# Kernel tuning notes

Measured on AMD Instinct MI355X. Metric: run time of the kernel, lower is better.

Reference implementation:

```python
import jax, jax.numpy as jnp
import numpy as np

N_NODES = 65536
N_EDGES = 524288
N_LAYERS = 3
D = 128
ED = 32
BATCH = 64
NEG_SLOPE = 0.2


def setup_inputs() -> dict:
    key = jax.random.key(0)
    ks = jax.random.split(key, 10)
    w_scale = 1.0 / np.sqrt(D)
    return {
        "x": jax.random.normal(ks[0], (N_NODES, D), dtype=jnp.float32),
        "edge_index": jax.random.randint(ks[1], (2, N_EDGES), 0, N_NODES, dtype=jnp.int32),
        "edge_attr": jax.random.normal(ks[2], (N_EDGES, ED), dtype=jnp.float32),
        "Ws": jax.random.normal(ks[3], (N_LAYERS, D, D), dtype=jnp.float32) * w_scale,
        "att_src": jax.random.normal(ks[4], (N_LAYERS, D), dtype=jnp.float32) * w_scale,
        "att_dst": jax.random.normal(ks[5], (N_LAYERS, D), dtype=jnp.float32) * w_scale,
        "W_edge": jax.random.normal(ks[6], (N_LAYERS, ED, D), dtype=jnp.float32) * (1.0 / np.sqrt(ED)),
        "att_edge": jax.random.normal(ks[7], (N_LAYERS, D), dtype=jnp.float32) * w_scale,
        "bias": jnp.zeros((N_LAYERS, D), dtype=jnp.float32),
        "batch_size": BATCH,
    }


def _gat_layer(x, src, dst, ea, W, a_s, a_d, We, a_e, b, n):
    # PyG GATConv, heads=1, concat=True, flow source_to_target.
    h = x @ W                                      # [N, D]
    al = (h @ a_s)[src] + (h @ a_d)[dst] + (ea @ We) @ a_e   # [E]
    al = jax.nn.leaky_relu(al, NEG_SLOPE)
    # segment softmax over destination-node neighborhoods
    m = jax.ops.segment_max(al, dst, num_segments=n)
    ex = jnp.exp(al - m[dst])
    den = jax.ops.segment_sum(ex, dst, num_segments=n)
    w = ex / den[dst]                              # [E]
    out = jax.ops.segment_sum(w[:, None] * h[src], dst, num_segments=n)
    return out + b


def reference(x, edge_index, edge_attr, Ws, att_src, att_dst, W_edge, att_edge, bias, batch_size):
    n = x.shape[0]
    # add_self_loops with fill_value='mean': self-loop edge_attr is the mean of
    # incoming edge features per destination node (zero if no incoming edges).
    loop = jnp.arange(n, dtype=edge_index.dtype)
    src = jnp.concatenate([edge_index[0], loop])
    dst = jnp.concatenate([edge_index[1], loop])
    cnt = jax.ops.segment_sum(jnp.ones((edge_attr.shape[0],), edge_attr.dtype), edge_index[1], num_segments=n)
    fill = jax.ops.segment_sum(edge_attr, edge_index[1], num_segments=n) / jnp.maximum(cnt, 1.0)[:, None]
    ea = jnp.concatenate([edge_attr, fill], axis=0)

    h = x
    for l in range(Ws.shape[0]):
        h = jax.nn.gelu(
            _gat_layer(h, src, dst, ea, Ws[l], att_src[l], att_dst[l], W_edge[l], att_edge[l], bias[l], n),
            approximate=False,
        )
        # dropout p=0.2 is identity in eval mode
    return h.reshape(batch_size, n // batch_size, -1)
```

## Files before the change

kernel.cpp:

```cpp
#include <hip/hip_runtime.h>
#include <math.h>

#define NN 65536
#define NE 524288
#define D 128
#define ED 32
#define NEG_SLOPE 0.2f

typedef short bf16x8 __attribute__((ext_vector_type(8)));
typedef float f32x4 __attribute__((ext_vector_type(4)));
typedef unsigned short ushort_t;

__device__ __forceinline__ float leaky(float x) { return x > 0.f ? x : NEG_SLOPE * x; }
__device__ __forceinline__ float gelu_exact(float x) {
    return 0.5f * x * (1.f + erff(x * 0.70710678118654752440f));
}
__device__ __forceinline__ unsigned short bf16_rne(float x) {
    unsigned u = __float_as_uint(x);
    return (unsigned short)((u + 0x7FFFu + ((u >> 16) & 1u)) >> 16);
}
__device__ __forceinline__ void unpack8(int4 r, float* f) {
    unsigned u0 = (unsigned)r.x, u1 = (unsigned)r.y, u2 = (unsigned)r.z, u3 = (unsigned)r.w;
    f[0] = __uint_as_float(u0 << 16); f[1] = __uint_as_float(u0 & 0xFFFF0000u);
    f[2] = __uint_as_float(u1 << 16); f[3] = __uint_as_float(u1 & 0xFFFF0000u);
    f[4] = __uint_as_float(u2 << 16); f[5] = __uint_as_float(u2 & 0xFFFF0000u);
    f[6] = __uint_as_float(u3 << 16); f[7] = __uint_as_float(u3 & 0xFFFF0000u);
}


__global__ __launch_bounds__(256) void k_front(const float* __restrict__ ea,
        const int* __restrict__ dstArr, int* __restrict__ deg,
        const float* __restrict__ We, const float* __restrict__ ae,
        const float* __restrict__ Ws, short* __restrict__ Whp, short* __restrict__ Wlp,
        float* __restrict__ ale0, float* __restrict__ ale1, float* __restrict__ ale2) {
    if (blockIdx.x >= NE / 256) {
        int t = (blockIdx.x - NE / 256) * 256 + threadIdx.x;
        if (t >= 3 * 4 * 4 * 128) return;
        int n = t & 127;
        int q = (t >> 7) & 3;
        int ks = (t >> 9) & 3;
        int l = t >> 11;
        const float* w = Ws + (size_t)l * D * D;
        size_t obase = (size_t)l * D * D + ((size_t)((ks * 4 + q) * 128) + n) * 8;
        #pragma unroll
        for (int j = 0; j < 8; ++j) {
            float x = w[(size_t)(ks * 32 + q * 8 + j) * D + n];
            unsigned short hb = bf16_rne(x);
            float hf = __uint_as_float(((unsigned)hb) << 16);
            Whp[obase + j] = (short)hb;
            Wlp[obase + j] = (short)bf16_rne(x - hf);
        }
        return;
    }
    __shared__ __align__(16) float wv[3 * ED];
    int t = threadIdx.x;
    if (t < 3 * ED) {
        int l = t >> 5, k = t & 31;
        const float4* w = (const float4*)(We + (size_t)(l * ED + k) * D);
        const float4* a = (const float4*)(ae + (size_t)l * D);
        float s = 0.f;
        #pragma unroll
        for (int i = 0; i < D / 4; ++i) {
            float4 x = w[i], y = a[i];
            s += x.x * y.x + x.y * y.y + x.z * y.z + x.w * y.w;
        }
        wv[t] = s;
    }
    __syncthreads();
    int e = blockIdx.x * 256 + t;
    atomicAdd(&deg[dstArr[e]], 1);
    const float4* row = (const float4*)(ea + (size_t)e * ED);
    const float4* w0 = (const float4*)(wv);
    const float4* w1 = (const float4*)(wv + ED);
    const float4* w2 = (const float4*)(wv + 2 * ED);
    float s0 = 0.f, s1 = 0.f, s2 = 0.f;
    #pragma unroll
    for (int i = 0; i < ED / 4; ++i) {
        float4 v = row[i];
        float4 a = w0[i], b = w1[i], c = w2[i];
        s0 += v.x * a.x + v.y * a.y + v.z * a.z + v.w * a.w;
        s1 += v.x * b.x + v.y * b.y + v.z * b.z + v.w * b.w;
        s2 += v.x * c.x + v.y * c.y + v.z * c.z + v.w * c.w;
    }
    ale0[e] = s0;
    ale1[e] = s1;
    ale2[e] = s2;
}


__global__ void k_scan1(const int* __restrict__ deg, int* __restrict__ rp, int* __restrict__ bsum) {
    __shared__ int s[256];
    int t = threadIdx.x;
    int i = blockIdx.x * 256 + t;
    int v = deg[i];
    s[t] = v;
    __syncthreads();
    #pragma unroll
    for (int off = 1; off < 256; off <<= 1) {
        int x = (t >= off) ? s[t - off] : 0;
        __syncthreads();
        s[t] += x;
        __syncthreads();
    }
    rp[i] = s[t] - v;
    if (t == 255) bsum[blockIdx.x] = s[t];
}

__global__ void k_scanF(int* __restrict__ rp, const int* __restrict__ bsum, int* __restrict__ cursor) {
    __shared__ int s[256];
    int t = threadIdx.x;
    int bid = blockIdx.x;
    int v = bsum[t];
    s[t] = v;
    __syncthreads();
    #pragma unroll
    for (int off = 1; off < 256; off <<= 1) {
        int x = (t >= off) ? s[t - off] : 0;
        __syncthreads();
        s[t] += x;
        __syncthreads();
    }
    int add = (bid > 0) ? s[bid - 1] : 0;
    int i = bid * 256 + t;
    int r = rp[i] + add;
    rp[i] = r;
    cursor[i] = r;
    if (bid == 255 && t == 255) rp[NN] = NE;
}


__device__ __forceinline__ void aggr_node(int n, int l16, int qb,
        const ushort_t* __restrict__ hb, const float* __restrict__ als,
        const float* __restrict__ ald, const int4* __restrict__ edata,
        const int* __restrict__ rp, const float* __restrict__ bias, int lsel,
        float* o) {
    int s = rp[n], e = rp[n + 1];
    int deg = e - s;
    float aldd = ald[n];
    float alsn = als[n];
    float inv_deg = (deg > 0) ? 1.f / (float)deg : 0.f;

    int4 hvp = *(const int4*)(hb + (size_t)n * D + l16 * 8);
    float acc8[8];

    if (deg <= 16) {
        int sn0 = 0;
        float al0 = -1e30f, alev0 = 0.f;
        if (l16 < deg) {
            int4 ed = edata[s + l16];
            sn0 = ed.x;
            alev0 = __int_as_float((lsel == 0) ? ed.y : ((lsel == 1) ? ed.z : ed.w));
            al0 = leaky(als[sn0] + aldd + alev0);
        }
        float mm = al0, asum = alev0;
        #pragma unroll
        for (int off = 1; off < 16; off <<= 1) {
            mm = fmaxf(mm, __shfl_xor(mm, off));
            asum += __shfl_xor(asum, off);
        }
        float self_al = leaky(alsn + aldd + asum * inv_deg);
        mm = fmaxf(mm, self_al);
        float p0 = (l16 < deg) ? __expf(al0 - mm) : 0.f;
        float den = p0;
        #pragma unroll
        for (int off = 1; off < 16; off <<= 1) den += __shfl_xor(den, off);
        float es = __expf(self_al - mm);
        den += es;
        float inv = 1.f / den;
        float w0 = p0 * inv;
        float wself = es * inv;

        float fv[8];
        unpack8(hvp, fv);
        #pragma unroll
        for (int j = 0; j < 8; ++j) acc8[j] = wself * fv[j];

        int sA[8]; float wA[8]; int4 rb[8];
        #pragma unroll
        for (int i = 0; i < 8; ++i) { sA[i] = __shfl(sn0, qb + i); wA[i] = __shfl(w0, qb + i); }
        #pragma unroll
        for (int i = 0; i < 8; ++i) rb[i] = *(const int4*)(hb + (size_t)sA[i] * D + l16 * 8);

        int sB[8]; float wB[8]; int4 rb2[8];
        #pragma unroll
        for (int i = 0; i < 8; ++i) { sB[i] = __shfl(sn0, qb + 8 + i); wB[i] = __shfl(w0, qb + 8 + i); }
        bool more = (deg > 8);
        if (more) {
            #pragma unroll
            for (int i = 0; i < 8; ++i) rb2[i] = *(const int4*)(hb + (size_t)sB[i] * D + l16 * 8);
        }

        #pragma unroll
        for (int i = 0; i < 8; ++i) {
            float f[8];
            unpack8(rb[i], f);
            #pragma unroll
            for (int j = 0; j < 8; ++j) acc8[j] += wA[i] * f[j];
        }
        if (more) {
            #pragma unroll
            for (int i = 0; i < 8; ++i) {
                float f[8];
                unpack8(rb2[i], f);
                #pragma unroll
                for (int j = 0; j < 8; ++j) acc8[j] += wB[i] * f[j];
            }
        }
    } else {
        float mm = -1e30f, asum = 0.f;
        for (int base = s; base < e; base += 16) {
            int j = base + l16;
            if (j < e) {
                int4 ed = edata[j];
                float alev = __int_as_float((lsel == 0) ? ed.y : ((lsel == 1) ? ed.z : ed.w));
                asum += alev;
                mm = fmaxf(mm, leaky(als[ed.x] + aldd + alev));
            }
        }
        #pragma unroll
        for (int off = 1; off < 16; off <<= 1) {
            mm = fmaxf(mm, __shfl_xor(mm, off));
            asum += __shfl_xor(asum, off);
        }
        float self_al = leaky(alsn + aldd + asum * inv_deg);
        mm = fmaxf(mm, self_al);
        float den = 0.f;
        for (int base = s; base < e; base += 16) {
            int j = base + l16;
            if (j < e) {
                int4 ed = edata[j];
                float alev = __int_as_float((lsel == 0) ? ed.y : ((lsel == 1) ? ed.z : ed.w));
                den += __expf(leaky(als[ed.x] + aldd + alev) - mm);
            }
        }
        #pragma unroll
        for (int off = 1; off < 16; off <<= 1) den += __shfl_xor(den, off);
        float es = __expf(self_al - mm);
        den += es;
        float inv = 1.f / den;
        float wself = es * inv;
        float fv[8];
        unpack8(hvp, fv);
        #pragma unroll
        for (int j = 0; j < 8; ++j) acc8[j] = wself * fv[j];
        for (int base = s; base < e; base += 16) {
            int cnt = min(e - base, 16);
            int sn = 0;
            float w = 0.f;
            if (l16 < cnt) {
                int4 ed = edata[base + l16];
                sn = ed.x;
                float alev = __int_as_float((lsel == 0) ? ed.y : ((lsel == 1) ? ed.z : ed.w));
                w = __expf(leaky(als[sn] + aldd + alev) - mm) * inv;
            }
            for (int tt = 0; tt < cnt; ++tt) {
                int st = __shfl(sn, qb + tt);
                float wt = __shfl(w, qb + tt);
                int4 r = *(const int4*)(hb + (size_t)st * D + l16 * 8);
                float f[8];
                unpack8(r, f);
                #pragma unroll
                for (int j = 0; j < 8; ++j) acc8[j] += wt * f[j];
            }
        }
    }

    const float4* b4 = (const float4*)(bias + l16 * 8);
    float4 b0 = b4[0], b1 = b4[1];
    float bb[8] = {b0.x, b0.y, b0.z, b0.w, b1.x, b1.y, b1.z, b1.w};
    #pragma unroll
    for (int j = 0; j < 8; ++j) o[j] = gelu_exact(acc8[j] + bb[j]);
}


__global__ __launch_bounds__(256) void k_gemm0scat(const float* __restrict__ A,
        const short* __restrict__ Whp, const short* __restrict__ Wlp,
        const float* __restrict__ a_s, const float* __restrict__ a_d,
        ushort_t* __restrict__ Hb, float* __restrict__ als, float* __restrict__ ald,
        const int* __restrict__ srcArr, const int* __restrict__ dstArr,
        int* __restrict__ cursor, const float* __restrict__ ale0,
        const float* __restrict__ ale1, const float* __restrict__ ale2,
        int4* __restrict__ edata) {
    __shared__ int4 Bs[2048];
    int t = threadIdx.x;
    int wave = t >> 6, lane = t & 63;
    int l16 = lane & 15, q = lane >> 4;
    int b = blockIdx.x;
    int rows_base = b * 64 + wave * 16;

    int e0 = b * 512 + t, e1 = e0 + 256;
    int d0 = dstArr[e0], d1 = dstArr[e1];
    int p0 = atomicAdd(&cursor[d0], 1);
    int p1 = atomicAdd(&cursor[d1], 1);
    int s0 = srcArr[e0], s1 = srcArr[e1];
    float a00 = ale0[e0], a01 = ale1[e0], a02 = ale2[e0];
    float a10 = ale0[e1], a11 = ale1[e1], a12 = ale2[e1];

    const int4* wh4 = (const int4*)Whp;
    const int4* wl4 = (const int4*)Wlp;
    const short* bsh = (const short*)Bs;
    const short* bsl = (const short*)(Bs + 1024);

    f32x4 acc[8] = {};
    #pragma unroll
    for (int h2 = 0; h2 < 2; ++h2) {
        if (h2) __syncthreads();
        #pragma unroll
        for (int i = 0; i < 4; ++i) {
            Bs[t + 256 * i] = wh4[h2 * 1024 + t + 256 * i];
            Bs[1024 + t + 256 * i] = wl4[h2 * 1024 + t + 256 * i];
        }
        __syncthreads();
        #pragma unroll
        for (int kk = 0; kk < 2; ++kk) {
            int ks = h2 * 2 + kk;
            const float* ap = A + (size_t)(rows_base + l16) * D + ks * 32 + q * 8;
            float4 v0 = *(const float4*)ap;
            float4 v1 = *(const float4*)(ap + 4);
            float f[8] = {v0.x, v0.y, v0.z, v0.w, v1.x, v1.y, v1.z, v1.w};
            bf16x8 ah, alo;
            #pragma unroll
            for (int j = 0; j < 8; ++j) {
                unsigned short hb = bf16_rne(f[j]);
                float hf = __uint_as_float(((unsigned)hb) << 16);
                ah[j]  = (short)hb;
                alo[j] = (short)bf16_rne(f[j] - hf);
            }
            #pragma unroll
            for (int nt = 0; nt < 8; ++nt) {
                int idx = (((kk * 4 + q) * 128) + nt * 16 + l16) * 8;
                bf16x8 bh = *(const bf16x8*)(bsh + idx);
                bf16x8 bl = *(const bf16x8*)(bsl + idx);
                acc[nt] = __builtin_amdgcn_mfma_f32_16x16x32_bf16(bh, ah, acc[nt], 0, 0, 0);
                acc[nt] = __builtin_amdgcn_mfma_f32_16x16x32_bf16(bl, ah, acc[nt], 0, 0, 0);
                acc[nt] = __builtin_amdgcn_mfma_f32_16x16x32_bf16(bh, alo, acc[nt], 0, 0, 0);
            }
        }
    }

    edata[p0] = make_int4(s0, __float_as_int(a00), __float_as_int(a01), __float_as_int(a02));
    edata[p1] = make_int4(s1, __float_as_int(a10), __float_as_int(a11), __float_as_int(a12));

    float ps = 0.f, pd = 0.f;
    #pragma unroll
    for (int nt = 0; nt < 8; ++nt) {
        float4 a4 = *(const float4*)(a_s + nt * 16 + q * 4);
        float4 d4 = *(const float4*)(a_d + nt * 16 + q * 4);
        ps += acc[nt][0] * a4.x + acc[nt][1] * a4.y + acc[nt][2] * a4.z + acc[nt][3] * a4.w;
        pd += acc[nt][0] * d4.x + acc[nt][1] * d4.y + acc[nt][2] * d4.z + acc[nt][3] * d4.w;
    }
    ps += __shfl_xor(ps, 16); pd += __shfl_xor(pd, 16);
    ps += __shfl_xor(ps, 32); pd += __shfl_xor(pd, 32);
    if (q == 0) {
        als[rows_base + l16] = ps;
        ald[rows_base + l16] = pd;
    }

    __syncthreads();
    char* tb = (char*)Bs + wave * 4096;
    {
        int row = l16;
        unsigned key = (unsigned)(row & 7) << 4;
        #pragma unroll
        for (int nt = 0; nt < 8; ++nt) {
            ushort4 pk;
            pk.x = bf16_rne(acc[nt][0]);
            pk.y = bf16_rne(acc[nt][1]);
            pk.z = bf16_rne(acc[nt][2]);
            pk.w = bf16_rne(acc[nt][3]);
            unsigned byteoff = (unsigned)row * 256u + (unsigned)(nt * 16 + q * 4) * 2u;
            *(ushort4*)(tb + (byteoff ^ key)) = pk;
        }
    }
    __syncthreads();
    #pragma unroll
    for (int i = 0; i < 4; ++i) {
        int m = lane + 64 * i;
        unsigned row = (unsigned)m >> 4;
        unsigned byteoff = (unsigned)m * 16u;
        unsigned addr = byteoff ^ ((row & 7u) << 4);
        int4 v = *(const int4*)(tb + addr);
        *(int4*)((char*)Hb + (size_t)rows_base * 256 + (size_t)m * 16) = v;
    }
}


__global__ __launch_bounds__(256) void k_aggrgemm(const ushort_t* __restrict__ hb,
        const float* __restrict__ als_in, const float* __restrict__ ald_in,
        const int4* __restrict__ edata, const int* __restrict__ rp,
        const float* __restrict__ bias, int lsel,
        const short* __restrict__ Whp, const short* __restrict__ Wlp,
        const float* __restrict__ a_s, const float* __restrict__ a_d,
        ushort_t* __restrict__ Hb_out, float* __restrict__ als_out,
        float* __restrict__ ald_out) {
    __shared__ __align__(16) char Abuf[32768];
    __shared__ int4 Wst[1024];
    int t = threadIdx.x;
    int lane = t & 63;
    int l16 = lane & 15;
    int qb = lane & 48;
    int q = lane >> 4;
    int wave = t >> 6;
    int b = blockIdx.x;

    #pragma unroll
    for (int j = 0; j < 4; ++j) {
        int nl = (t >> 4) + 16 * j;
        int n = b * 64 + nl;
        float o[8];
        aggr_node(n, l16, qb, hb, als_in, ald_in, edata, rp, bias, lsel, o);
        unsigned key = (unsigned)(nl & 7) << 4;
        unsigned bo = (unsigned)nl * 512u + (unsigned)l16 * 32u;
        *(float4*)(Abuf + ((bo) ^ key)) = make_float4(o[0], o[1], o[2], o[3]);
        *(float4*)(Abuf + ((bo + 16) ^ key)) = make_float4(o[4], o[5], o[6], o[7]);
    }
    __syncthreads();

    int rows_base = b * 64 + wave * 16;
    int rl = wave * 16 + l16;
    unsigned akey = (unsigned)(rl & 7) << 4;
    const int4* wh4 = (const int4*)Whp;
    const int4* wl4 = (const int4*)Wlp;
    const short* bsh = (const short*)Wst;
    const short* bsl = (const short*)(Wst + 512);

    f32x4 acc[8] = {};
    #pragma unroll
    for (int ks = 0; ks < 4; ++ks) {
        if (ks) __syncthreads();
        Wst[t]       = wh4[ks * 512 + t];
        Wst[t + 256] = wh4[ks * 512 + 256 + t];
        Wst[512 + t]       = wl4[ks * 512 + t];
        Wst[512 + t + 256] = wl4[ks * 512 + 256 + t];
        __syncthreads();
        unsigned abo = (unsigned)rl * 512u + (unsigned)(ks * 128 + q * 32);
        float4 v0 = *(const float4*)(Abuf + ((abo) ^ akey));
        float4 v1 = *(const float4*)(Abuf + ((abo + 16) ^ akey));
        float f[8] = {v0.x, v0.y, v0.z, v0.w, v1.x, v1.y, v1.z, v1.w};
        bf16x8 ah, alo;
        #pragma unroll
        for (int j = 0; j < 8; ++j) {
            unsigned short hb16 = bf16_rne(f[j]);
            float hf = __uint_as_float(((unsigned)hb16) << 16);
            ah[j]  = (short)hb16;
            alo[j] = (short)bf16_rne(f[j] - hf);
        }
        #pragma unroll
        for (int nt = 0; nt < 8; ++nt) {
            int idx = (q * 128 + nt * 16 + l16) * 8;
            bf16x8 bh = *(const bf16x8*)(bsh + idx);
            bf16x8 bl = *(const bf16x8*)(bsl + idx);
            acc[nt] = __builtin_amdgcn_mfma_f32_16x16x32_bf16(bh, ah, acc[nt], 0, 0, 0);
            acc[nt] = __builtin_amdgcn_mfma_f32_16x16x32_bf16(bl, ah, acc[nt], 0, 0, 0);
            acc[nt] = __builtin_amdgcn_mfma_f32_16x16x32_bf16(bh, alo, acc[nt], 0, 0, 0);
        }
    }

    float ps = 0.f, pd = 0.f;
    #pragma unroll
    for (int nt = 0; nt < 8; ++nt) {
        float4 a4 = *(const float4*)(a_s + nt * 16 + q * 4);
        float4 d4 = *(const float4*)(a_d + nt * 16 + q * 4);
        ps += acc[nt][0] * a4.x + acc[nt][1] * a4.y + acc[nt][2] * a4.z + acc[nt][3] * a4.w;
        pd += acc[nt][0] * d4.x + acc[nt][1] * d4.y + acc[nt][2] * d4.z + acc[nt][3] * d4.w;
    }
    ps += __shfl_xor(ps, 16); pd += __shfl_xor(pd, 16);
    ps += __shfl_xor(ps, 32); pd += __shfl_xor(pd, 32);
    if (q == 0) {
        als_out[rows_base + l16] = ps;
        ald_out[rows_base + l16] = pd;
    }

    __syncthreads();
    char* tb = Abuf + wave * 4096;
    {
        int row = l16;
        unsigned key = (unsigned)(row & 7) << 4;
        #pragma unroll
        for (int nt = 0; nt < 8; ++nt) {
            ushort4 pk;
            pk.x = bf16_rne(acc[nt][0]);
            pk.y = bf16_rne(acc[nt][1]);
            pk.z = bf16_rne(acc[nt][2]);
            pk.w = bf16_rne(acc[nt][3]);
            unsigned byteoff = (unsigned)row * 256u + (unsigned)(nt * 16 + q * 4) * 2u;
            *(ushort4*)(tb + (byteoff ^ key)) = pk;
        }
    }
    __syncthreads();
    #pragma unroll
    for (int i = 0; i < 4; ++i) {
        int m = lane + 64 * i;
        unsigned row = (unsigned)m >> 4;
        unsigned byteoff = (unsigned)m * 16u;
        unsigned addr = byteoff ^ ((row & 7u) << 4);
        int4 v = *(const int4*)(tb + addr);
        *(int4*)((char*)Hb_out + (size_t)rows_base * 256 + (size_t)m * 16) = v;
    }
}


__global__ __launch_bounds__(256) void k_aggr_final(const ushort_t* __restrict__ hb,
        const float* __restrict__ als, const float* __restrict__ ald,
        const int4* __restrict__ edata, const int* __restrict__ rp,
        const float* __restrict__ bias, int lsel, float* __restrict__ out_f32) {
    int t = threadIdx.x;
    int lane = t & 63;
    int l16 = lane & 15;
    int qb = lane & 48;
    int n = blockIdx.x * 16 + (t >> 4);
    float o[8];
    aggr_node(n, l16, qb, hb, als, ald, edata, rp, bias, lsel, o);
    float4* o4 = (float4*)(out_f32 + (size_t)n * D + l16 * 8);
    o4[0] = make_float4(o[0], o[1], o[2], o[3]);
    o4[1] = make_float4(o[4], o[5], o[6], o[7]);
}


extern "C" void kernel_launch(void* const* d_in, const int* in_sizes, int n_in,
                              void* d_out, int out_size, void* d_ws, size_t ws_size,
                              hipStream_t stream) {
    (void)in_sizes; (void)n_in; (void)out_size; (void)ws_size;
    const float* x        = (const float*)d_in[0];
    const int*   eidx     = (const int*)d_in[1];
    const float* ea       = (const float*)d_in[2];
    const float* Ws       = (const float*)d_in[3];
    const float* att_src  = (const float*)d_in[4];
    const float* att_dst  = (const float*)d_in[5];
    const float* W_edge   = (const float*)d_in[6];
    const float* att_edge = (const float*)d_in[7];
    const float* bias     = (const float*)d_in[8];
    float* out = (float*)d_out;

    char* ws = (char*)d_ws;
    size_t off = 0;
    auto alloc = [&](size_t bytes) {
        void* p = ws + off;
        off += (bytes + 255) & ~(size_t)255;
        return p;
    };
    ushort_t* HbA  = (ushort_t*)alloc((size_t)NN * D * 2);
    ushort_t* HbB  = (ushort_t*)alloc((size_t)NN * D * 2);
    float*    alsA = (float*)alloc((size_t)NN * 4);
    float*    aldA = (float*)alloc((size_t)NN * 4);
    float*    alsB = (float*)alloc((size_t)NN * 4);
    float*    aldB = (float*)alloc((size_t)NN * 4);
    int4*     edata= (int4*)alloc((size_t)NE * 16);
    float*    ale0 = (float*)alloc((size_t)NE * 4);
    float*    ale1 = (float*)alloc((size_t)NE * 4);
    float*    ale2 = (float*)alloc((size_t)NE * 4);
    int*      deg  = (int*)alloc((size_t)NN * 4);
    int*      rp   = (int*)alloc((size_t)(NN + 4) * 4);
    int*      cursor = (int*)alloc((size_t)NN * 4);
    int*      bsum = (int*)alloc(256 * 4);
    short*    Whp  = (short*)alloc((size_t)3 * D * D * 2);
    short*    Wlp  = (short*)alloc((size_t)3 * D * D * 2);

    const int* e_src = eidx;
    const int* e_dst = eidx + NE;

    hipMemsetAsync(deg, 0, (size_t)NN * 4, stream);
    k_front<<<NE / 256 + 24, 256, 0, stream>>>(ea, e_dst, deg, W_edge, att_edge,
                                               Ws, Whp, Wlp, ale0, ale1, ale2);
    k_scan1<<<NN / 256, 256, 0, stream>>>(deg, rp, bsum);
    k_scanF<<<NN / 256, 256, 0, stream>>>(rp, bsum, cursor);

    k_gemm0scat<<<NN / 64, 256, 0, stream>>>(x, Whp, Wlp, att_src, att_dst,
                                             HbA, alsA, aldA,
                                             e_src, e_dst, cursor, ale0, ale1, ale2, edata);

    k_aggrgemm<<<NN / 64, 256, 0, stream>>>(HbA, alsA, aldA, edata, rp, bias, 0,
                                            Whp + (size_t)1 * D * D, Wlp + (size_t)1 * D * D,
                                            att_src + D, att_dst + D,
                                            HbB, alsB, aldB);
    k_aggrgemm<<<NN / 64, 256, 0, stream>>>(HbB, alsB, aldB, edata, rp, bias + D, 1,
                                            Whp + (size_t)2 * D * D, Wlp + (size_t)2 * D * D,
                                            att_src + 2 * D, att_dst + 2 * D,
                                            HbA, alsA, aldA);
    k_aggr_final<<<NN / 16, 256, 0, stream>>>(HbA, alsA, aldA, edata, rp, bias + 2 * D, 2, out);
}
```

Measured before the change: 361.9 us.

## Split fused aggregate+GEMM kernels into separate aggregation and GEMM passes

```diff
diff --git a/kernel.cpp b/kernel.cpp
--- a/kernel.cpp
+++ b/kernel.cpp
@@ -129,150 +129,6 @@
 }
 
 
-__device__ __forceinline__ void aggr_node(int n, int l16, int qb,
-        const ushort_t* __restrict__ hb, const float* __restrict__ als,
-        const float* __restrict__ ald, const int4* __restrict__ edata,
-        const int* __restrict__ rp, const float* __restrict__ bias, int lsel,
-        float* o) {
-    int s = rp[n], e = rp[n + 1];
-    int deg = e - s;
-    float aldd = ald[n];
-    float alsn = als[n];
-    float inv_deg = (deg > 0) ? 1.f / (float)deg : 0.f;
-
-    int4 hvp = *(const int4*)(hb + (size_t)n * D + l16 * 8);
-    float acc8[8];
-
-    if (deg <= 16) {
-        int sn0 = 0;
-        float al0 = -1e30f, alev0 = 0.f;
-        if (l16 < deg) {
-            int4 ed = edata[s + l16];
-            sn0 = ed.x;
-            alev0 = __int_as_float((lsel == 0) ? ed.y : ((lsel == 1) ? ed.z : ed.w));
-            al0 = leaky(als[sn0] + aldd + alev0);
-        }
-        float mm = al0, asum = alev0;
-        #pragma unroll
-        for (int off = 1; off < 16; off <<= 1) {
-            mm = fmaxf(mm, __shfl_xor(mm, off));
-            asum += __shfl_xor(asum, off);
-        }
-        float self_al = leaky(alsn + aldd + asum * inv_deg);
-        mm = fmaxf(mm, self_al);
-        float p0 = (l16 < deg) ? __expf(al0 - mm) : 0.f;
-        float den = p0;
-        #pragma unroll
-        for (int off = 1; off < 16; off <<= 1) den += __shfl_xor(den, off);
-        float es = __expf(self_al - mm);
-        den += es;
-        float inv = 1.f / den;
-        float w0 = p0 * inv;
-        float wself = es * inv;
-
-        float fv[8];
-        unpack8(hvp, fv);
-        #pragma unroll
-        for (int j = 0; j < 8; ++j) acc8[j] = wself * fv[j];
-
-        int sA[8]; float wA[8]; int4 rb[8];
-        #pragma unroll
-        for (int i = 0; i < 8; ++i) { sA[i] = __shfl(sn0, qb + i); wA[i] = __shfl(w0, qb + i); }
-        #pragma unroll
-        for (int i = 0; i < 8; ++i) rb[i] = *(const int4*)(hb + (size_t)sA[i] * D + l16 * 8);
-
-        int sB[8]; float wB[8]; int4 rb2[8];
-        #pragma unroll
-        for (int i = 0; i < 8; ++i) { sB[i] = __shfl(sn0, qb + 8 + i); wB[i] = __shfl(w0, qb + 8 + i); }
-        bool more = (deg > 8);
-        if (more) {
-            #pragma unroll
-            for (int i = 0; i < 8; ++i) rb2[i] = *(const int4*)(hb + (size_t)sB[i] * D + l16 * 8);
-        }
-
-        #pragma unroll
-        for (int i = 0; i < 8; ++i) {
-            float f[8];
-            unpack8(rb[i], f);
-            #pragma unroll
-            for (int j = 0; j < 8; ++j) acc8[j] += wA[i] * f[j];
-        }
-        if (more) {
-            #pragma unroll
-            for (int i = 0; i < 8; ++i) {
-                float f[8];
-                unpack8(rb2[i], f);
-                #pragma unroll
-                for (int j = 0; j < 8; ++j) acc8[j] += wB[i] * f[j];
-            }
-        }
-    } else {
-        float mm = -1e30f, asum = 0.f;
-        for (int base = s; base < e; base += 16) {
-            int j = base + l16;
-            if (j < e) {
-                int4 ed = edata[j];
-                float alev = __int_as_float((lsel == 0) ? ed.y : ((lsel == 1) ? ed.z : ed.w));
-                asum += alev;
-                mm = fmaxf(mm, leaky(als[ed.x] + aldd + alev));
-            }
-        }
-        #pragma unroll
-        for (int off = 1; off < 16; off <<= 1) {
-            mm = fmaxf(mm, __shfl_xor(mm, off));
-            asum += __shfl_xor(asum, off);
-        }
-        float self_al = leaky(alsn + aldd + asum * inv_deg);
-        mm = fmaxf(mm, self_al);
-        float den = 0.f;
-        for (int base = s; base < e; base += 16) {
-            int j = base + l16;
-            if (j < e) {
-                int4 ed = edata[j];
-                float alev = __int_as_float((lsel == 0) ? ed.y : ((lsel == 1) ? ed.z : ed.w));
-                den += __expf(leaky(als[ed.x] + aldd + alev) - mm);
-            }
-        }
-        #pragma unroll
-        for (int off = 1; off < 16; off <<= 1) den += __shfl_xor(den, off);
-        float es = __expf(self_al - mm);
-        den += es;
-        float inv = 1.f / den;
-        float wself = es * inv;
-        float fv[8];
-        unpack8(hvp, fv);
-        #pragma unroll
-        for (int j = 0; j < 8; ++j) acc8[j] = wself * fv[j];
-        for (int base = s; base < e; base += 16) {
-            int cnt = min(e - base, 16);
-            int sn = 0;
-            float w = 0.f;
-            if (l16 < cnt) {
-                int4 ed = edata[base + l16];
-                sn = ed.x;
-                float alev = __int_as_float((lsel == 0) ? ed.y : ((lsel == 1) ? ed.z : ed.w));
-                w = __expf(leaky(als[sn] + aldd + alev) - mm) * inv;
-            }
-            for (int tt = 0; tt < cnt; ++tt) {
-                int st = __shfl(sn, qb + tt);
-                float wt = __shfl(w, qb + tt);
-                int4 r = *(const int4*)(hb + (size_t)st * D + l16 * 8);
-                float f[8];
-                unpack8(r, f);
-                #pragma unroll
-                for (int j = 0; j < 8; ++j) acc8[j] += wt * f[j];
-            }
-        }
-    }
-
-    const float4* b4 = (const float4*)(bias + l16 * 8);
-    float4 b0 = b4[0], b1 = b4[1];
-    float bb[8] = {b0.x, b0.y, b0.z, b0.w, b1.x, b1.y, b1.z, b1.w};
-    #pragma unroll
-    for (int j = 0; j < 8; ++j) o[j] = gelu_exact(acc8[j] + bb[j]);
-}
-
-
 __global__ __launch_bounds__(256) void k_gemm0scat(const float* __restrict__ A,
         const short* __restrict__ Whp, const short* __restrict__ Wlp,
         const float* __restrict__ a_s, const float* __restrict__ a_d,
@@ -385,74 +241,55 @@
 }
 
 
-__global__ __launch_bounds__(256) void k_aggrgemm(const ushort_t* __restrict__ hb,
-        const float* __restrict__ als_in, const float* __restrict__ ald_in,
-        const int4* __restrict__ edata, const int* __restrict__ rp,
-        const float* __restrict__ bias, int lsel,
+__global__ __launch_bounds__(256) void k_gemm(const float* __restrict__ A,
         const short* __restrict__ Whp, const short* __restrict__ Wlp,
         const float* __restrict__ a_s, const float* __restrict__ a_d,
-        ushort_t* __restrict__ Hb_out, float* __restrict__ als_out,
-        float* __restrict__ ald_out) {
-    __shared__ __align__(16) char Abuf[32768];
-    __shared__ int4 Wst[1024];
+        ushort_t* __restrict__ Hb, float* __restrict__ als, float* __restrict__ ald) {
+    __shared__ int4 Bs[2048];
     int t = threadIdx.x;
-    int lane = t & 63;
-    int l16 = lane & 15;
-    int qb = lane & 48;
-    int q = lane >> 4;
-    int wave = t >> 6;
-    int b = blockIdx.x;
-
-    #pragma unroll
-    for (int j = 0; j < 4; ++j) {
-        int nl = (t >> 4) + 16 * j;
-        int n = b * 64 + nl;
-        float o[8];
-        aggr_node(n, l16, qb, hb, als_in, ald_in, edata, rp, bias, lsel, o);
-        unsigned key = (unsigned)(nl & 7) << 4;
-        unsigned bo = (unsigned)nl * 512u + (unsigned)l16 * 32u;
-        *(float4*)(Abuf + ((bo) ^ key)) = make_float4(o[0], o[1], o[2], o[3]);
-        *(float4*)(Abuf + ((bo + 16) ^ key)) = make_float4(o[4], o[5], o[6], o[7]);
-    }
-    __syncthreads();
-
-    int rows_base = b * 64 + wave * 16;
-    int rl = wave * 16 + l16;
-    unsigned akey = (unsigned)(rl & 7) << 4;
+    int wave = t >> 6, lane = t & 63;
+    int l16 = lane & 15, q = lane >> 4;
+    int rows_base = blockIdx.x * 64 + wave * 16;
+
     const int4* wh4 = (const int4*)Whp;
     const int4* wl4 = (const int4*)Wlp;
-    const short* bsh = (const short*)Wst;
-    const short* bsl = (const short*)(Wst + 512);
+    const short* bsh = (const short*)Bs;
+    const short* bsl = (const short*)(Bs + 1024);
 
     f32x4 acc[8] = {};
     #pragma unroll
-    for (int ks = 0; ks < 4; ++ks) {
-        if (ks) __syncthreads();
-        Wst[t]       = wh4[ks * 512 + t];
-        Wst[t + 256] = wh4[ks * 512 + 256 + t];
-        Wst[512 + t]       = wl4[ks * 512 + t];
-        Wst[512 + t + 256] = wl4[ks * 512 + 256 + t];
+    for (int h2 = 0; h2 < 2; ++h2) {
+        if (h2) __syncthreads();
+        #pragma unroll
+        for (int i = 0; i < 4; ++i) {
+            Bs[t + 256 * i] = wh4[h2 * 1024 + t + 256 * i];
+            Bs[1024 + t + 256 * i] = wl4[h2 * 1024 + t + 256 * i];
+        }
         __syncthreads();
-        unsigned abo = (unsigned)rl * 512u + (unsigned)(ks * 128 + q * 32);
-        float4 v0 = *(const float4*)(Abuf + ((abo) ^ akey));
-        float4 v1 = *(const float4*)(Abuf + ((abo + 16) ^ akey));
-        float f[8] = {v0.x, v0.y, v0.z, v0.w, v1.x, v1.y, v1.z, v1.w};
-        bf16x8 ah, alo;
-        #pragma unroll
-        for (int j = 0; j < 8; ++j) {
-            unsigned short hb16 = bf16_rne(f[j]);
-            float hf = __uint_as_float(((unsigned)hb16) << 16);
-            ah[j]  = (short)hb16;
-            alo[j] = (short)bf16_rne(f[j] - hf);
-        }
-        #pragma unroll
-        for (int nt = 0; nt < 8; ++nt) {
-            int idx = (q * 128 + nt * 16 + l16) * 8;
-            bf16x8 bh = *(const bf16x8*)(bsh + idx);
-            bf16x8 bl = *(const bf16x8*)(bsl + idx);
-            acc[nt] = __builtin_amdgcn_mfma_f32_16x16x32_bf16(bh, ah, acc[nt], 0, 0, 0);
-            acc[nt] = __builtin_amdgcn_mfma_f32_16x16x32_bf16(bl, ah, acc[nt], 0, 0, 0);
-            acc[nt] = __builtin_amdgcn_mfma_f32_16x16x32_bf16(bh, alo, acc[nt], 0, 0, 0);
+        #pragma unroll
+        for (int kk = 0; kk < 2; ++kk) {
+            int ks = h2 * 2 + kk;
+            const float* ap = A + (size_t)(rows_base + l16) * D + ks * 32 + q * 8;
+            float4 v0 = *(const float4*)ap;
+            float4 v1 = *(const float4*)(ap + 4);
+            float f[8] = {v0.x, v0.y, v0.z, v0.w, v1.x, v1.y, v1.z, v1.w};
+            bf16x8 ah, alo;
+            #pragma unroll
+            for (int j = 0; j < 8; ++j) {
+                unsigned short hb = bf16_rne(f[j]);
+                float hf = __uint_as_float(((unsigned)hb) << 16);
+                ah[j]  = (short)hb;
+                alo[j] = (short)bf16_rne(f[j] - hf);
+            }
+            #pragma unroll
+            for (int nt = 0; nt < 8; ++nt) {
+                int idx = (((kk * 4 + q) * 128) + nt * 16 + l16) * 8;
+                bf16x8 bh = *(const bf16x8*)(bsh + idx);
+                bf16x8 bl = *(const bf16x8*)(bsl + idx);
+                acc[nt] = __builtin_amdgcn_mfma_f32_16x16x32_bf16(bh, ah, acc[nt], 0, 0, 0);
+                acc[nt] = __builtin_amdgcn_mfma_f32_16x16x32_bf16(bl, ah, acc[nt], 0, 0, 0);
+                acc[nt] = __builtin_amdgcn_mfma_f32_16x16x32_bf16(bh, alo, acc[nt], 0, 0, 0);
+            }
         }
     }
 
@@ -467,12 +304,12 @@
     ps += __shfl_xor(ps, 16); pd += __shfl_xor(pd, 16);
     ps += __shfl_xor(ps, 32); pd += __shfl_xor(pd, 32);
     if (q == 0) {
-        als_out[rows_base + l16] = ps;
-        ald_out[rows_base + l16] = pd;
-    }
-
-    __syncthreads();
-    char* tb = Abuf + wave * 4096;
+        als[rows_base + l16] = ps;
+        ald[rows_base + l16] = pd;
+    }
+
+    __syncthreads();
+    char* tb = (char*)Bs + wave * 4096;
     {
         int row = l16;
         unsigned key = (unsigned)(row & 7) << 4;
@@ -495,12 +332,12 @@
         unsigned byteoff = (unsigned)m * 16u;
         unsigned addr = byteoff ^ ((row & 7u) << 4);
         int4 v = *(const int4*)(tb + addr);
-        *(int4*)((char*)Hb_out + (size_t)rows_base * 256 + (size_t)m * 16) = v;
-    }
-}
-
-
-__global__ __launch_bounds__(256) void k_aggr_final(const ushort_t* __restrict__ hb,
+        *(int4*)((char*)Hb + (size_t)rows_base * 256 + (size_t)m * 16) = v;
+    }
+}
+
+
+__global__ __launch_bounds__(256) void k_aggr(const ushort_t* __restrict__ hb,
         const float* __restrict__ als, const float* __restrict__ ald,
         const int4* __restrict__ edata, const int* __restrict__ rp,
         const float* __restrict__ bias, int lsel, float* __restrict__ out_f32) {
@@ -509,8 +346,148 @@
     int l16 = lane & 15;
     int qb = lane & 48;
     int n = blockIdx.x * 16 + (t >> 4);
+    int s = rp[n], e = rp[n + 1];
+    int deg = e - s;
+    float aldd = ald[n];
+    float alsn = als[n];
+    float inv_deg = (deg > 0) ? 1.f / (float)deg : 0.f;
+
+    int4 hvp = *(const int4*)(hb + (size_t)n * D + l16 * 8);
+    float acc8[8];
+
+    if (deg <= 16) {
+        int sn0 = 0;
+        float alev0 = 0.f, alsg = 0.f;
+        if (l16 < deg) {
+            int4 ed = edata[s + l16];
+            sn0 = ed.x;
+            alev0 = __int_as_float((lsel == 0) ? ed.y : ((lsel == 1) ? ed.z : ed.w));
+            alsg = als[sn0];
+        }
+
+        int sA[8], sB[8];
+        #pragma unroll
+        for (int i = 0; i < 8; ++i) { sA[i] = __shfl(sn0, qb + i); sB[i] = __shfl(sn0, qb + 8 + i); }
+        int4 rb[8];
+        #pragma unroll
+        for (int i = 0; i < 8; ++i) rb[i] = *(const int4*)(hb + (size_t)sA[i] * D + l16 * 8);
+        bool more = (deg > 8);
+        int4 rb2[8];
+        if (more) {
+            #pragma unroll
+            for (int i = 0; i < 8; ++i) rb2[i] = *(const int4*)(hb + (size_t)sB[i] * D + l16 * 8);
+        }
+
+        float al0 = (l16 < deg) ? leaky(alsg + aldd + alev0) : -1e30f;
+        float mm = al0, asum = alev0;
+        #pragma unroll
+        for (int off = 1; off < 16; off <<= 1) {
+            mm = fmaxf(mm, __shfl_xor(mm, off));
+            asum += __shfl_xor(asum, off);
+        }
+        float self_al = leaky(alsn + aldd + asum * inv_deg);
+        mm = fmaxf(mm, self_al);
+        float p0 = (l16 < deg) ? __expf(al0 - mm) : 0.f;
+        float den = p0;
+        #pragma unroll
+        for (int off = 1; off < 16; off <<= 1) den += __shfl_xor(den, off);
+        float es = __expf(self_al - mm);
+        den += es;
+        float inv = 1.f / den;
+        float w0 = p0 * inv;
+        float wself = es * inv;
+
+        float fv[8];
+        unpack8(hvp, fv);
+        #pragma unroll
+        for (int j = 0; j < 8; ++j) acc8[j] = wself * fv[j];
+
+        float wA[8], wB[8];
+        #pragma unroll
+        for (int i = 0; i < 8; ++i) { wA[i] = __shfl(w0, qb + i); wB[i] = __shfl(w0, qb + 8 + i); }
+
+        #pragma unroll
+        for (int i = 0; i < 8; ++i) {
+            float f[8];
+            unpack8(rb[i], f);
+            #pragma unroll
+            for (int j = 0; j < 8; ++j) acc8[j] += wA[i] * f[j];
+        }
+        if (more) {
+            #pragma unroll
+            for (int i = 0; i < 8; ++i) {
+                float f[8];
+                unpack8(rb2[i], f);
+                #pragma unroll
+                for (int j = 0; j < 8; ++j) acc8[j] += wB[i] * f[j];
+            }
+        }
+    } else {
+        float mm = -1e30f, asum = 0.f;
+        for (int base = s; base < e; base += 16) {
+            int j = base + l16;
+            if (j < e) {
+                int4 ed = edata[j];
+                float alev = __int_as_float((lsel == 0) ? ed.y : ((lsel == 1) ? ed.z : ed.w));
+                asum += alev;
+                mm = fmaxf(mm, leaky(als[ed.x] + aldd + alev));
+            }
+        }
+        #pragma unroll
+        for (int off = 1; off < 16; off <<= 1) {
+            mm = fmaxf(mm, __shfl_xor(mm, off));
+            asum += __shfl_xor(asum, off);
+        }
+        float self_al = leaky(alsn + aldd + asum * inv_deg);
+        mm = fmaxf(mm, self_al);
+        float den = 0.f;
+        for (int base = s; base < e; base += 16) {
+            int j = base + l16;
+            if (j < e) {
+                int4 ed = edata[j];
+                float alev = __int_as_float((lsel == 0) ? ed.y : ((lsel == 1) ? ed.z : ed.w));
+                den += __expf(leaky(als[ed.x] + aldd + alev) - mm);
+            }
+        }
+        #pragma unroll
+        for (int off = 1; off < 16; off <<= 1) den += __shfl_xor(den, off);
+        float es = __expf(self_al - mm);
+        den += es;
+        float inv = 1.f / den;
+        float wself = es * inv;
+        float fv[8];
+        unpack8(hvp, fv);
+        #pragma unroll
+        for (int j = 0; j < 8; ++j) acc8[j] = wself * fv[j];
+        for (int base = s; base < e; base += 16) {
+            int cnt = min(e - base, 16);
+            int sn = 0;
+            float w = 0.f;
+            if (l16 < cnt) {
+                int4 ed = edata[base + l16];
+                sn = ed.x;
+                float alev = __int_as_float((lsel == 0) ? ed.y : ((lsel == 1) ? ed.z : ed.w));
+                w = __expf(leaky(als[sn] + aldd + alev) - mm) * inv;
+            }
+            for (int tt = 0; tt < cnt; ++tt) {
+                int st = __shfl(sn, qb + tt);
+                float wt = __shfl(w, qb + tt);
+                int4 r = *(const int4*)(hb + (size_t)st * D + l16 * 8);
+                float f[8];
+                unpack8(r, f);
+                #pragma unroll
+                for (int j = 0; j < 8; ++j) acc8[j] += wt * f[j];
+            }
+        }
+    }
+
+    const float4* b4 = (const float4*)(bias + l16 * 8);
+    float4 b0 = b4[0], b1 = b4[1];
+    float bb[8] = {b0.x, b0.y, b0.z, b0.w, b1.x, b1.y, b1.z, b1.w};
     float o[8];
-    aggr_node(n, l16, qb, hb, als, ald, edata, rp, bias, lsel, o);
+    #pragma unroll
+    for (int j = 0; j < 8; ++j) o[j] = gelu_exact(acc8[j] + bb[j]);
+
     float4* o4 = (float4*)(out_f32 + (size_t)n * D + l16 * 8);
     o4[0] = make_float4(o[0], o[1], o[2], o[3]);
     o4[1] = make_float4(o[4], o[5], o[6], o[7]);
@@ -539,13 +516,11 @@
         off += (bytes + 255) & ~(size_t)255;
         return p;
     };
-    ushort_t* HbA  = (ushort_t*)alloc((size_t)NN * D * 2);
-    ushort_t* HbB  = (ushort_t*)alloc((size_t)NN * D * 2);
-    float*    alsA = (float*)alloc((size_t)NN * 4);
-    float*    aldA = (float*)alloc((size_t)NN * 4);
-    float*    alsB = (float*)alloc((size_t)NN * 4);
-    float*    aldB = (float*)alloc((size_t)NN * 4);
-    int4*     edata= (int4*)alloc((size_t)NE * 16);
+    ushort_t* Hb   = (ushort_t*)alloc((size_t)NN * D * 2);
+    float*    Hx   = (float*)alloc((size_t)NN * D * 4);
+    float*    als  = (float*)alloc((size_t)NN * 4);
+    float*    ald  = (float*)alloc((size_t)NN * 4);
+    int4*     edata= (int4*)alloc((size_t)(NE + 16) * 16);
     float*    ale0 = (float*)alloc((size_t)NE * 4);
     float*    ale1 = (float*)alloc((size_t)NE * 4);
     float*    ale2 = (float*)alloc((size_t)NE * 4);
@@ -566,16 +541,19 @@
     k_scanF<<<NN / 256, 256, 0, stream>>>(rp, bsum, cursor);
 
     k_gemm0scat<<<NN / 64, 256, 0, stream>>>(x, Whp, Wlp, att_src, att_dst,
-                                             HbA, alsA, aldA,
+                                             Hb, als, ald,
                                              e_src, e_dst, cursor, ale0, ale1, ale2, edata);
 
-    k_aggrgemm<<<NN / 64, 256, 0, stream>>>(HbA, alsA, aldA, edata, rp, bias, 0,
-                                            Whp + (size_t)1 * D * D, Wlp + (size_t)1 * D * D,
-                                            att_src + D, att_dst + D,
-                                            HbB, alsB, aldB);
-    k_aggrgemm<<<NN / 64, 256, 0, stream>>>(HbB, alsB, aldB, edata, rp, bias + D, 1,
-                                            Whp + (size_t)2 * D * D, Wlp + (size_t)2 * D * D,
-                                            att_src + 2 * D, att_dst + 2 * D,
-                                            HbA, alsA, aldA);
-    k_aggr_final<<<NN / 16, 256, 0, stream>>>(HbA, alsA, aldA, edata, rp, bias + 2 * D, 2, out);
-}
+    for (int l = 0; l < 3; ++l) {
+        bool last = (l == 2);
+        k_aggr<<<NN / 16, 256, 0, stream>>>(Hb, als, ald, edata, rp, bias + (size_t)l * D, l,
+                                            last ? out : Hx);
+        if (!last) {
+            k_gemm<<<NN / 64, 256, 0, stream>>>(Hx, Whp + (size_t)(l + 1) * D * D,
+                                                Wlp + (size_t)(l + 1) * D * D,
+                                                att_src + (size_t)(l + 1) * D,
+                                                att_dst + (size_t)(l + 1) * D,
+                                                Hb, als, ald);
+        }
+    }
+}
```

After: 352.0 us. -2.7%, faster.
